# Kernel tuning notes

Measured on AMD Instinct MI355X. Metric: run time of the kernel, lower is better.

## Reference

```python
import jax, jax.numpy as jnp
import numpy as np
import math

B, T, N, D = 2, 2048, 16, 128


def setup_inputs() -> dict:
    key = jax.random.key(0)
    ks = jax.random.split(key, 9)
    s = 1.0 / math.sqrt(D)
    return {
        "x": jax.random.normal(ks[0], (B, T, N, D), dtype=jnp.float32),
        "wq": jax.random.normal(ks[1], (D, D), dtype=jnp.float32) * s,
        "bq": jax.random.normal(ks[2], (D,), dtype=jnp.float32) * 0.02,
        "wk": jax.random.normal(ks[3], (D, D), dtype=jnp.float32) * s,
        "bk": jax.random.normal(ks[4], (D,), dtype=jnp.float32) * 0.02,
        "wv": jax.random.normal(ks[5], (D, D), dtype=jnp.float32) * s,
        "bv": jax.random.normal(ks[6], (D,), dtype=jnp.float32) * 0.02,
        "wp": jax.random.normal(ks[7], (D, D), dtype=jnp.float32) * s,
        "bp": jax.random.normal(ks[8], (D,), dtype=jnp.float32) * 0.02,
    }


def reference(x, wq, bq, wk, bk, wv, bv, wp, bp):
    # x: (B, T, N, D); per-head Linear projections (torch y = x @ W.T + b)
    d = x.shape[-1]
    q = jnp.einsum("btnd,ed->btne", x, wq) + bq  # (B,T,N,D)
    k = jnp.einsum("btnd,ed->btne", x, wk) + bk
    v = jnp.einsum("btnd,ed->btne", x, wv) + bv
    scale = 1.0 / jnp.sqrt(jnp.asarray(d, dtype=x.dtype))
    # scores: (B, N, T, T)
    scores = jnp.einsum("btnd,bsnd->bnts", q, k) * scale
    t = scores.shape[-1]
    causal = jnp.tril(jnp.ones((t, t), dtype=bool))  # (T,T)
    scores = jnp.where(causal[None, None], scores, jnp.asarray(-jnp.inf, scores.dtype))
    w = jax.nn.softmax(scores, axis=-1)
    att = jnp.einsum("bnts,bsnd->btnd", w, v)  # (B,T,N,D)
    out = jnp.einsum("btnd,ed->btne", att, wp) + bp
    return out
```

## Files before the change

kernel.cpp:

```cpp
#include <hip/hip_runtime.h>
#include <cmath>

#define BB 2
#define TT 2048
#define NN 16
#define DD 128
#define NROWS (BB*TT*NN)
#define PLANE (TT*DD)
#define KP 132
#define VP 68

typedef unsigned short u16;
typedef unsigned int   u32;
typedef __attribute__((ext_vector_type(8)))  short s8v;
typedef __attribute__((ext_vector_type(16))) float vf16;

__device__ u16 g_Q [(size_t)NROWS * DD];
__device__ u16 g_K [(size_t)NROWS * DD];
__device__ u16 g_V [(size_t)NROWS * DD];
__device__ u16 g_VT[(size_t)NROWS * DD];

__device__ __forceinline__ u16 f2bf(float f) {
    return (u16)((__float_as_uint(f) + 0x8000u) >> 16);
}
__device__ __forceinline__ u32 pk2(float a, float b) {
    return ((__float_as_uint(a) + 0x8000u) >> 16)
         | ((__float_as_uint(b) + 0x8000u) & 0xFFFF0000u);
}
__device__ __forceinline__ void st8(u16* p, const float4& a, const float4& b) {
    uint2 lo, hi;
    lo.x = pk2(a.x, a.y); lo.y = pk2(a.z, a.w);
    hi.x = pk2(b.x, b.y); hi.y = pk2(b.z, b.w);
    *(uint2*)p       = lo;
    *(uint2*)(p + 4) = hi;
}
__device__ __forceinline__ s8v ld8(const u16* p) {
    short4 a = *(const short4*)p;
    short4 b = *(const short4*)(p + 4);
    return (s8v){a.x, a.y, a.z, a.w, b.x, b.y, b.z, b.w};
}

__global__ __launch_bounds__(256)
void qkv_proj_kernel(const float* __restrict__ x,
                     const float* __restrict__ Wq, const float* __restrict__ Bq,
                     const float* __restrict__ Wk, const float* __restrict__ Bk,
                     const float* __restrict__ Wv, const float* __restrict__ Bv)
{
    __shared__ u16 Xs[128*KP];
    __shared__ u16 Ws[128*KP];

    const int t  = threadIdx.x;
    const int r0 = blockIdx.x * 128;
    const float4* xsrc = (const float4*)(x + (size_t)r0*DD);

    #pragma unroll
    for (int it = 0; it < 8; ++it) {
        int i = t + 256*it;
        int e = i >> 4, c8 = i & 15;
        st8(&Xs[e*KP + c8*8], xsrc[2*i], xsrc[2*i + 1]);
    }
    #pragma unroll
    for (int it = 0; it < 8; ++it) {
        int i = t + 256*it;
        int e = i >> 4, c8 = i & 15;
        st8(&Ws[e*KP + c8*8], ((const float4*)Wq)[2*i], ((const float4*)Wq)[2*i + 1]);
    }
    __syncthreads();

    const int w   = t >> 6;
    const int l31 = t & 31;
    const int q2  = (t >> 5) & 1;

    s8v af[8];
    #pragma unroll
    for (int s = 0; s < 8; ++s)
        af[s] = ld8(&Xs[(w*32 + l31)*KP + s*16 + q2*8]);

    #pragma unroll
    for (int wsel = 0; wsel < 3; ++wsel) {
        const float* Bi = (wsel == 0) ? Bq : (wsel == 1) ? Bk : Bv;
        u16*         Ot = (wsel == 0) ? g_Q : (wsel == 1) ? g_K : g_V;

        vf16 acc[4];
        #pragma unroll
        for (int et = 0; et < 4; ++et)
            #pragma unroll
            for (int i = 0; i < 16; ++i) acc[et][i] = 0.f;

        #pragma unroll
        for (int s = 0; s < 8; ++s) {
            #pragma unroll
            for (int et = 0; et < 4; ++et) {
                s8v bf = ld8(&Ws[(et*32 + l31)*KP + s*16 + q2*8]);
                acc[et] = __builtin_amdgcn_mfma_f32_32x32x16_bf16(af[s], bf, acc[et], 0, 0, 0);
            }
        }

        float bb[4];
        #pragma unroll
        for (int et = 0; et < 4; ++et) bb[et] = Bi[et*32 + l31];

        #pragma unroll
        for (int r = 0; r < 16; ++r) {
            int rl = (r & 3) + 8*(r >> 2) + 4*q2;
            int rg = r0 + w*32 + rl;
            int b = rg >> 15, rem = rg & 32767;
            int tt = rem >> 4, n = rem & 15;
            size_t orow = (size_t)((b*NN + n)*TT + tt) * DD;
            #pragma unroll
            for (int et = 0; et < 4; ++et)
                Ot[orow + et*32 + l31] = f2bf(acc[et][r] + bb[et]);
        }

        if (wsel < 2) {
            const float* Wn = (wsel == 0) ? Wk : Wv;
            __syncthreads();
            #pragma unroll
            for (int it = 0; it < 8; ++it) {
                int i = t + 256*it;
                int e = i >> 4, c8 = i & 15;
                st8(&Ws[e*KP + c8*8], ((const float4*)Wn)[2*i], ((const float4*)Wn)[2*i + 1]);
            }
            __syncthreads();
        }
    }
}

__global__ __launch_bounds__(256)
void out_proj_kernel(const float* __restrict__ W, const float* __restrict__ Bi,
                     float* __restrict__ out)
{
    __shared__ u16 Ws[128*KP];

    const int t  = threadIdx.x;
    const int r0 = blockIdx.x * 128;

    #pragma unroll
    for (int it = 0; it < 8; ++it) {
        int i = t + 256*it;
        int e = i >> 4, c8 = i & 15;
        st8(&Ws[e*KP + c8*8], ((const float4*)W)[2*i], ((const float4*)W)[2*i + 1]);
    }

    const int w   = t >> 6;
    const int l31 = t & 31;
    const int q2  = (t >> 5) & 1;

    s8v af[8];
    {
        const u16* src = g_Q + (size_t)(r0 + w*32 + l31)*DD;
        #pragma unroll
        for (int s = 0; s < 8; ++s)
            af[s] = *(const s8v*)&src[s*16 + q2*8];
    }
    __syncthreads();

    vf16 acc[4];
    #pragma unroll
    for (int et = 0; et < 4; ++et)
        #pragma unroll
        for (int i = 0; i < 16; ++i) acc[et][i] = 0.f;

    #pragma unroll
    for (int s = 0; s < 8; ++s) {
        #pragma unroll
        for (int et = 0; et < 4; ++et) {
            s8v bf = ld8(&Ws[(et*32 + l31)*KP + s*16 + q2*8]);
            acc[et] = __builtin_amdgcn_mfma_f32_32x32x16_bf16(af[s], bf, acc[et], 0, 0, 0);
        }
    }

    float bb[4];
    #pragma unroll
    for (int et = 0; et < 4; ++et) bb[et] = Bi[et*32 + l31];

    #pragma unroll
    for (int r = 0; r < 16; ++r) {
        int rl = (r & 3) + 8*(r >> 2) + 4*q2;
        int rg = r0 + w*32 + rl;
        int b = rg >> 15, rem = rg & 32767;
        int n = rem >> 11, tt = rem & 2047;
        size_t orow = (size_t)((b*TT + tt)*NN + n) * DD;
        #pragma unroll
        for (int et = 0; et < 4; ++et)
            out[orow + et*32 + l31] = acc[et][r] + bb[et];
    }
}

__global__ __launch_bounds__(256)
void vtrans_kernel()
{
    const int t   = threadIdx.x;
    const int blk = blockIdx.x;
    const int pl  = blk >> 7;
    const int seg = blk & 127;
    const size_t plane = (size_t)pl * PLANE;
    const int w = t >> 6, lane = t & 63;
    const int d   = (w & 1)*64 + lane;
    const int tt0 = seg*16 + (w >> 1)*8;

    const u16* src = g_V + plane + (size_t)tt0*DD + d;
    u16 e[8];
    #pragma unroll
    for (int i = 0; i < 8; ++i) e[i] = src[(size_t)i*DD];
    uint4 pk;
    pk.x = (u32)e[0] | ((u32)e[1] << 16);
    pk.y = (u32)e[2] | ((u32)e[3] << 16);
    pk.z = (u32)e[4] | ((u32)e[5] << 16);
    pk.w = (u32)e[6] | ((u32)e[7] << 16);
    *(uint4*)&g_VT[plane + (size_t)d*TT + tt0] = pk;
}

__global__ __launch_bounds__(256, 2)
void attn_kernel()
{
    __shared__ u16 Ks[64*KP];
    __shared__ u16 Vt[128*VP];

    const int t   = threadIdx.x;
    const int grp = blockIdx.x >> 5;
    const int bn  = blockIdx.x & 31;
    const int qt  = (grp < 8) ? (15 - grp) : (grp - 8);
    const int q0  = qt * 128;
    const size_t plane = (size_t)bn * PLANE;
    const u16* Kg = g_K  + plane;
    const u16* Vg = g_VT + plane;

    const int w      = t >> 6;
    const int lane   = t & 63;
    const int lane31 = lane & 31;
    const int q2     = lane >> 5;
    const int qband  = q0 + 32*w;
    const int qrow   = qband + lane31;

    s8v qf[8];
    {
        const u16* Qg = g_Q + plane + (size_t)qrow * DD;
        #pragma unroll
        for (int s = 0; s < 8; ++s)
            qf[s] = *(const s8v*)&Qg[s*16 + q2*8];
    }

    vf16 accO[4];
    #pragma unroll
    for (int dt = 0; dt < 4; ++dt)
        #pragma unroll
        for (int i = 0; i < 16; ++i) accO[dt][i] = 0.f;

    float mrow = -INFINITY, lrow = 0.f;
    const float sc2 = 0.08838834764831845f * 1.4426950408889634f;

    const int nkt = 2*qt + 2;

    uint4 pk[4], pv[4];
    #pragma unroll
    for (int c = 0; c < 4; ++c) {
        int j = t + 256*c;
        int kr = j >> 4, kc = j & 15;
        pk[c] = *(const uint4*)&Kg[kr*DD + kc*8];
        int vr = j >> 3, vc = j & 7;
        pv[c] = *(const uint4*)&Vg[(size_t)vr*TT + vc*8];
    }

    for (int kt = 0; kt < nkt; ++kt) {
        const int k0 = kt*64;
        __syncthreads();
        #pragma unroll
        for (int c = 0; c < 4; ++c) {
            int j = t + 256*c;
            int kr = j >> 4, kc = j & 15;
            uint2 a, b;
            a.x = pk[c].x; a.y = pk[c].y; b.x = pk[c].z; b.y = pk[c].w;
            *(uint2*)&Ks[kr*KP + kc*8]     = a;
            *(uint2*)&Ks[kr*KP + kc*8 + 4] = b;
            int vr = j >> 3, vc = j & 7;
            a.x = pv[c].x; a.y = pv[c].y; b.x = pv[c].z; b.y = pv[c].w;
            *(uint2*)&Vt[vr*VP + vc*8]     = a;
            *(uint2*)&Vt[vr*VP + vc*8 + 4] = b;
        }
        __syncthreads();

        if (kt + 1 < nkt) {
            const u16* Kg2 = Kg + (size_t)(k0 + 64)*DD;
            const u16* Vg2 = Vg + (k0 + 64);
            #pragma unroll
            for (int c = 0; c < 4; ++c) {
                int j = t + 256*c;
                int kr = j >> 4, kc = j & 15;
                pk[c] = *(const uint4*)&Kg2[kr*DD + kc*8];
                int vr = j >> 3, vc = j & 7;
                pv[c] = *(const uint4*)&Vg2[(size_t)vr*TT + vc*8];
            }
        }

        if (k0 > qband + 31) continue;

        vf16 accS[2];
        #pragma unroll
        for (int kk = 0; kk < 2; ++kk)
            #pragma unroll
            for (int i = 0; i < 16; ++i) accS[kk][i] = 0.f;
        #pragma unroll
        for (int s = 0; s < 8; ++s) {
            #pragma unroll
            for (int kk = 0; kk < 2; ++kk) {
                s8v a = ld8(&Ks[(kk*32 + lane31)*KP + s*16 + q2*8]);
                accS[kk] = __builtin_amdgcn_mfma_f32_32x32x16_bf16(a, qf[s], accS[kk], 0, 0, 0);
            }
        }

        float p[2][16];
        const bool tail = (k0 + 63 > qband);
        #pragma unroll
        for (int kk = 0; kk < 2; ++kk)
            #pragma unroll
            for (int r = 0; r < 16; ++r) {
                float sv = accS[kk][r] * sc2;
                if (tail) {
                    int keyg = k0 + kk*32 + (r & 3) + 8*(r >> 2) + 4*q2;
                    if (keyg > qrow) sv = -INFINITY;
                }
                p[kk][r] = sv;
            }

        float vmax = -INFINITY;
        #pragma unroll
        for (int kk = 0; kk < 2; ++kk)
            #pragma unroll
            for (int r = 0; r < 16; ++r) vmax = fmaxf(vmax, p[kk][r]);
        vmax = fmaxf(vmax, __shfl_xor(vmax, 32));
        float mold = mrow;
        float mnew = fmaxf(mold, vmax);
        float alpha = __builtin_amdgcn_exp2f(mold - mnew);
        mrow = mnew;
        float ls = 0.f;
        #pragma unroll
        for (int kk = 0; kk < 2; ++kk)
            #pragma unroll
            for (int r = 0; r < 16; ++r) {
                float e = __builtin_amdgcn_exp2f(p[kk][r] - mnew);
                p[kk][r] = e;
                ls += e;
            }
        ls += __shfl_xor(ls, 32);
        lrow = lrow*alpha + ls;

        if (__any(mnew > mold)) {
            float ar[16];
            #pragma unroll
            for (int r = 0; r < 16; ++r)
                ar[r] = __shfl(alpha, (r & 3) + 8*(r >> 2) + 4*q2);
            #pragma unroll
            for (int dt = 0; dt < 4; ++dt)
                #pragma unroll
                for (int r = 0; r < 16; ++r) accO[dt][r] *= ar[r];
        }

        s8v pf[4];
        #pragma unroll
        for (int tau = 0; tau < 4; ++tau) {
            int kk = tau >> 1, rb = (tau & 1)*8;
            s8v v;
            #pragma unroll
            for (int j = 0; j < 8; ++j)
                v[j] = (short)(__float_as_uint(p[kk][rb + j]) >> 16);
            pf[tau] = v;
        }

        #pragma unroll
        for (int dt = 0; dt < 4; ++dt) {
            const u16* vp = &Vt[(dt*32 + lane31)*VP];
            #pragma unroll
            for (int tau = 0; tau < 4; ++tau) {
                const u16* q = vp + 16*tau + 4*q2;
                short4 lo = *(const short4*)q;
                short4 hi = *(const short4*)(q + 8);
                s8v bvv = {lo.x, lo.y, lo.z, lo.w, hi.x, hi.y, hi.z, hi.w};
                accO[dt] = __builtin_amdgcn_mfma_f32_32x32x16_bf16(pf[tau], bvv, accO[dt], 0, 0, 0);
            }
        }
    }

    float inv = 1.0f / lrow;
    #pragma unroll
    for (int r = 0; r < 16; ++r) {
        int rl = (r & 3) + 8*(r >> 2) + 4*q2;
        float ir = __shfl(inv, rl);
        u16* op = g_Q + plane + (size_t)(qband + rl)*DD;
        #pragma unroll
        for (int dt = 0; dt < 4; ++dt)
            op[dt*32 + lane31] = f2bf(accO[dt][r] * ir);
    }
}

extern "C" void kernel_launch(void* const* d_in, const int* in_sizes, int n_in,
                              void* d_out, int out_size, void* d_ws, size_t ws_size,
                              hipStream_t stream)
{
    const float* x  = (const float*)d_in[0];
    const float* wq = (const float*)d_in[1];
    const float* bq = (const float*)d_in[2];
    const float* wk = (const float*)d_in[3];
    const float* bk = (const float*)d_in[4];
    const float* wv = (const float*)d_in[5];
    const float* bv = (const float*)d_in[6];
    const float* wp = (const float*)d_in[7];
    const float* bp = (const float*)d_in[8];
    float* out = (float*)d_out;
    (void)d_ws; (void)ws_size;

    dim3 blk(256);
    qkv_proj_kernel<<<dim3(NROWS/128), blk, 0, stream>>>(
        x, wq, bq, wk, bk, wv, bv);
    vtrans_kernel<<<dim3(BB*NN*128), blk, 0, stream>>>();
    attn_kernel<<<dim3(BB*NN*(TT/128)), blk, 0, stream>>>();
    out_proj_kernel<<<dim3(NROWS/128), blk, 0, stream>>>(wp, bp, out);
}
```

Measured before the change: 208.0 us.

## Balance causal attention work with split-KV pairing, fuse V transpose, coalesce stores

Attention blocks now pair a heavy and a light query tile and split the heavy tile's KV range across two blocks, so every block does 17 KV tiles. Partial results (O, m, l) go to global scratch and a new combine kernel merges them. The V transpose moves into the QKV projection through shared memory, which removes a kernel and the g_V buffer. The Q/K and output projection stores are staged through LDS for coalesced writes. The trade-off is extra float partial traffic, an added launch for the combine step, and more LDS use in out_proj.

```diff
diff --git a/kernel.cpp b/kernel.cpp
--- a/kernel.cpp
+++ b/kernel.cpp
@@ -17,8 +17,10 @@
 
 __device__ u16 g_Q [(size_t)NROWS * DD];
 __device__ u16 g_K [(size_t)NROWS * DD];
-__device__ u16 g_V [(size_t)NROWS * DD];
 __device__ u16 g_VT[(size_t)NROWS * DD];
+__device__ float g_pO[2][256][128*128];
+__device__ float g_pm[2][256][128];
+__device__ float g_pl[2][256][128];
 
 __device__ __forceinline__ u16 f2bf(float f) {
     return (u16)((__float_as_uint(f) + 0x8000u) >> 16);
@@ -58,11 +60,6 @@
         int i = t + 256*it;
         int e = i >> 4, c8 = i & 15;
         st8(&Xs[e*KP + c8*8], xsrc[2*i], xsrc[2*i + 1]);
-    }
-    #pragma unroll
-    for (int it = 0; it < 8; ++it) {
-        int i = t + 256*it;
-        int e = i >> 4, c8 = i & 15;
         st8(&Ws[e*KP + c8*8], ((const float4*)Wq)[2*i], ((const float4*)Wq)[2*i + 1]);
     }
     __syncthreads();
@@ -79,7 +76,6 @@
     #pragma unroll
     for (int wsel = 0; wsel < 3; ++wsel) {
         const float* Bi = (wsel == 0) ? Bq : (wsel == 1) ? Bk : Bv;
-        u16*         Ot = (wsel == 0) ? g_Q : (wsel == 1) ? g_K : g_V;
 
         vf16 acc[4];
         #pragma unroll
@@ -100,16 +96,59 @@
         #pragma unroll
         for (int et = 0; et < 4; ++et) bb[et] = Bi[et*32 + l31];
 
-        #pragma unroll
-        for (int r = 0; r < 16; ++r) {
-            int rl = (r & 3) + 8*(r >> 2) + 4*q2;
-            int rg = r0 + w*32 + rl;
+        __syncthreads();
+        if (wsel < 2) {
+            #pragma unroll
+            for (int et = 0; et < 4; ++et)
+                #pragma unroll
+                for (int r = 0; r < 16; ++r) {
+                    int rl = (r & 3) + 8*(r >> 2) + 4*q2;
+                    Ws[(w*32 + rl)*KP + et*32 + l31] = f2bf(acc[et][r] + bb[et]);
+                }
+        } else {
+            #pragma unroll
+            for (int et = 0; et < 4; ++et)
+                #pragma unroll
+                for (int r = 0; r < 16; ++r) {
+                    int rl = (r & 3) + 8*(r >> 2) + 4*q2;
+                    Ws[(et*32 + l31)*KP + w*32 + rl] = f2bf(acc[et][r] + bb[et]);
+                }
+        }
+        __syncthreads();
+
+        if (wsel < 2) {
+            u16* Ot = (wsel == 0) ? g_Q : g_K;
+            int row = t >> 1, half = t & 1;
+            int rg = r0 + row;
             int b = rg >> 15, rem = rg & 32767;
             int tt = rem >> 4, n = rem & 15;
-            size_t orow = (size_t)((b*NN + n)*TT + tt) * DD;
-            #pragma unroll
-            for (int et = 0; et < 4; ++et)
-                Ot[orow + et*32 + l31] = f2bf(acc[et][r] + bb[et]);
+            u16* dst = Ot + (size_t)((b*NN + n)*TT + tt)*DD + half*64;
+            const u16* src = &Ws[row*KP + half*64];
+            #pragma unroll
+            for (int j = 0; j < 8; ++j) {
+                uint2 a = ((const uint2*)src)[2*j];
+                uint2 c = ((const uint2*)src)[2*j + 1];
+                uint4 v; v.x = a.x; v.y = a.y; v.z = c.x; v.w = c.y;
+                ((uint4*)dst)[j] = v;
+            }
+        } else {
+            int b  = r0 >> 15;
+            int t0 = (r0 & 32767) >> 4;
+            #pragma unroll
+            for (int it = 0; it < 8; ++it) {
+                int idx = t + 256*it;
+                int n = idx >> 7, d = idx & 127;
+                u16 e[8];
+                #pragma unroll
+                for (int ti = 0; ti < 8; ++ti)
+                    e[ti] = Ws[d*KP + ti*16 + n];
+                uint4 pkv;
+                pkv.x = (u32)e[0] | ((u32)e[1] << 16);
+                pkv.y = (u32)e[2] | ((u32)e[3] << 16);
+                pkv.z = (u32)e[4] | ((u32)e[5] << 16);
+                pkv.w = (u32)e[6] | ((u32)e[7] << 16);
+                *(uint4*)&g_VT[(size_t)(b*NN + n)*PLANE + (size_t)d*TT + t0] = pkv;
+            }
         }
 
         if (wsel < 2) {
@@ -130,7 +169,8 @@
 void out_proj_kernel(const float* __restrict__ W, const float* __restrict__ Bi,
                      float* __restrict__ out)
 {
-    __shared__ u16 Ws[128*KP];
+    __shared__ u16   Ws[128*KP];
+    __shared__ float Cs[128*66];
 
     const int t  = threadIdx.x;
     const int r0 = blockIdx.x * 128;
@@ -174,41 +214,36 @@
     #pragma unroll
     for (int et = 0; et < 4; ++et) bb[et] = Bi[et*32 + l31];
 
-    #pragma unroll
-    for (int r = 0; r < 16; ++r) {
-        int rl = (r & 3) + 8*(r >> 2) + 4*q2;
-        int rg = r0 + w*32 + rl;
-        int b = rg >> 15, rem = rg & 32767;
-        int n = rem >> 11, tt = rem & 2047;
-        size_t orow = (size_t)((b*TT + tt)*NN + n) * DD;
-        #pragma unroll
-        for (int et = 0; et < 4; ++et)
-            out[orow + et*32 + l31] = acc[et][r] + bb[et];
-    }
-}
-
-__global__ __launch_bounds__(256)
-void vtrans_kernel()
-{
-    const int t   = threadIdx.x;
-    const int blk = blockIdx.x;
-    const int pl  = blk >> 7;
-    const int seg = blk & 127;
-    const size_t plane = (size_t)pl * PLANE;
-    const int w = t >> 6, lane = t & 63;
-    const int d   = (w & 1)*64 + lane;
-    const int tt0 = seg*16 + (w >> 1)*8;
-
-    const u16* src = g_V + plane + (size_t)tt0*DD + d;
-    u16 e[8];
-    #pragma unroll
-    for (int i = 0; i < 8; ++i) e[i] = src[(size_t)i*DD];
-    uint4 pk;
-    pk.x = (u32)e[0] | ((u32)e[1] << 16);
-    pk.y = (u32)e[2] | ((u32)e[3] << 16);
-    pk.z = (u32)e[4] | ((u32)e[5] << 16);
-    pk.w = (u32)e[6] | ((u32)e[7] << 16);
-    *(uint4*)&g_VT[plane + (size_t)d*TT + tt0] = pk;
+    const int row  = t >> 1;
+    const int seg  = t & 1;
+    int rg = r0 + row;
+    int b = rg >> 15, rem = rg & 32767;
+    int n = rem >> 11, tt = rem & 2047;
+    float* orow = out + (size_t)((b*TT + tt)*NN + n)*DD;
+
+    #pragma unroll
+    for (int h = 0; h < 2; ++h) {
+        #pragma unroll
+        for (int e2 = 0; e2 < 2; ++e2) {
+            int et = 2*h + e2;
+            #pragma unroll
+            for (int r = 0; r < 16; ++r) {
+                int rl = (r & 3) + 8*(r >> 2) + 4*q2;
+                Cs[(w*32 + rl)*66 + e2*32 + l31] = acc[et][r] + bb[et];
+            }
+        }
+        __syncthreads();
+        {
+            const float* src = &Cs[row*66 + seg*32];
+            float* dst = orow + h*64 + seg*32;
+            #pragma unroll
+            for (int j = 0; j < 16; ++j) {
+                float2 v = ((const float2*)src)[j];
+                ((float2*)dst)[j] = v;
+            }
+        }
+        __syncthreads();
+    }
 }
 
 __global__ __launch_bounds__(256, 2)
@@ -217,11 +252,16 @@
     __shared__ u16 Ks[64*KP];
     __shared__ u16 Vt[128*VP];
 
-    const int t   = threadIdx.x;
-    const int grp = blockIdx.x >> 5;
-    const int bn  = blockIdx.x & 31;
-    const int qt  = (grp < 8) ? (15 - grp) : (grp - 8);
-    const int q0  = qt * 128;
+    const int t    = threadIdx.x;
+    const int pid  = blockIdx.x;
+    const int bn   = pid & 31;
+    const int sid  = (pid >> 5) & 1;
+    const int g    = pid >> 6;
+    const int qt_h = 15 - g;
+    const int nkt_h = 2*qt_h + 2;
+    const int qt_l = g;
+    const int hidx = g*32 + bn;
+
     const size_t plane = (size_t)bn * PLANE;
     const u16* Kg = g_K  + plane;
     const u16* Vg = g_VT + plane;
@@ -230,8 +270,9 @@
     const int lane   = t & 63;
     const int lane31 = lane & 31;
     const int q2     = lane >> 5;
-    const int qband  = q0 + 32*w;
-    const int qrow   = qband + lane31;
+
+    int qband = qt_h*128 + 32*w;
+    int qrow  = qband + lane31;
 
     s8v qf[8];
     {
@@ -250,20 +291,57 @@
     float mrow = -INFINITY, lrow = 0.f;
     const float sc2 = 0.08838834764831845f * 1.4426950408889634f;
 
-    const int nkt = 2*qt + 2;
+    const int ph1n = (sid == 0) ? 17 : (nkt_h - 17);
+
+    auto K0 = [&](int i) -> int {
+        if (sid == 0) return i*64;
+        return (i < ph1n) ? (17 + i)*64 : (i - ph1n)*64;
+    };
 
     uint4 pk[4], pv[4];
-    #pragma unroll
-    for (int c = 0; c < 4; ++c) {
-        int j = t + 256*c;
-        int kr = j >> 4, kc = j & 15;
-        pk[c] = *(const uint4*)&Kg[kr*DD + kc*8];
-        int vr = j >> 3, vc = j & 7;
-        pv[c] = *(const uint4*)&Vg[(size_t)vr*TT + vc*8];
-    }
-
-    for (int kt = 0; kt < nkt; ++kt) {
-        const int k0 = kt*64;
+    {
+        const u16* Kg2 = Kg + (size_t)K0(0)*DD;
+        const u16* Vg2 = Vg + K0(0);
+        #pragma unroll
+        for (int c = 0; c < 4; ++c) {
+            int j = t + 256*c;
+            int kr = j >> 4, kc = j & 15;
+            pk[c] = *(const uint4*)&Kg2[kr*DD + kc*8];
+            int vr = j >> 3, vc = j & 7;
+            pv[c] = *(const uint4*)&Vg2[(size_t)vr*TT + vc*8];
+        }
+    }
+
+    for (int i = 0; i < 17; ++i) {
+        const int k0 = K0(i);
+
+        if (sid == 1 && i == ph1n) {
+            if (lane < 32) {
+                g_pm[1][hidx][32*w + lane31] = mrow;
+                g_pl[1][hidx][32*w + lane31] = lrow;
+            }
+            float* po = &g_pO[1][hidx][0];
+            #pragma unroll
+            for (int r = 0; r < 16; ++r) {
+                int rl = (r & 3) + 8*(r >> 2) + 4*q2;
+                float* dst = po + (32*w + rl)*128;
+                #pragma unroll
+                for (int dt = 0; dt < 4; ++dt)
+                    dst[dt*32 + lane31] = accO[dt][r];
+            }
+            qband = qt_l*128 + 32*w;
+            qrow  = qband + lane31;
+            const u16* Qg = g_Q + plane + (size_t)qrow * DD;
+            #pragma unroll
+            for (int s = 0; s < 8; ++s)
+                qf[s] = *(const s8v*)&Qg[s*16 + q2*8];
+            #pragma unroll
+            for (int dt = 0; dt < 4; ++dt)
+                #pragma unroll
+                for (int r = 0; r < 16; ++r) accO[dt][r] = 0.f;
+            mrow = -INFINITY; lrow = 0.f;
+        }
+
         __syncthreads();
         #pragma unroll
         for (int c = 0; c < 4; ++c) {
@@ -280,9 +358,10 @@
         }
         __syncthreads();
 
-        if (kt + 1 < nkt) {
-            const u16* Kg2 = Kg + (size_t)(k0 + 64)*DD;
-            const u16* Vg2 = Vg + (k0 + 64);
+        if (i + 1 < 17) {
+            const int kn = K0(i + 1);
+            const u16* Kg2 = Kg + (size_t)kn*DD;
+            const u16* Vg2 = Vg + kn;
             #pragma unroll
             for (int c = 0; c < 4; ++c) {
                 int j = t + 256*c;
@@ -299,7 +378,7 @@
         #pragma unroll
         for (int kk = 0; kk < 2; ++kk)
             #pragma unroll
-            for (int i = 0; i < 16; ++i) accS[kk][i] = 0.f;
+            for (int i2 = 0; i2 < 16; ++i2) accS[kk][i2] = 0.f;
         #pragma unroll
         for (int s = 0; s < 8; ++s) {
             #pragma unroll
@@ -381,15 +460,68 @@
         }
     }
 
-    float inv = 1.0f / lrow;
-    #pragma unroll
-    for (int r = 0; r < 16; ++r) {
-        int rl = (r & 3) + 8*(r >> 2) + 4*q2;
-        float ir = __shfl(inv, rl);
-        u16* op = g_Q + plane + (size_t)(qband + rl)*DD;
-        #pragma unroll
-        for (int dt = 0; dt < 4; ++dt)
-            op[dt*32 + lane31] = f2bf(accO[dt][r] * ir);
+    if (sid == 0) {
+        if (lane < 32) {
+            g_pm[0][hidx][32*w + lane31] = mrow;
+            g_pl[0][hidx][32*w + lane31] = lrow;
+        }
+        float* po = &g_pO[0][hidx][0];
+        #pragma unroll
+        for (int r = 0; r < 16; ++r) {
+            int rl = (r & 3) + 8*(r >> 2) + 4*q2;
+            float* dst = po + (32*w + rl)*128;
+            #pragma unroll
+            for (int dt = 0; dt < 4; ++dt)
+                dst[dt*32 + lane31] = accO[dt][r];
+        }
+    } else {
+        float inv = 1.0f / lrow;
+        #pragma unroll
+        for (int r = 0; r < 16; ++r) {
+            int rl = (r & 3) + 8*(r >> 2) + 4*q2;
+            float ir = __shfl(inv, rl);
+            u16* op = g_Q + plane + (size_t)(qband + rl)*DD;
+            #pragma unroll
+            for (int dt = 0; dt < 4; ++dt)
+                op[dt*32 + lane31] = f2bf(accO[dt][r] * ir);
+        }
+    }
+}
+
+__global__ __launch_bounds__(256)
+void combine_kernel()
+{
+    const int hidx = blockIdx.x;
+    const int g    = hidx >> 5;
+    const int bn   = hidx & 31;
+    const int qt_h = 15 - g;
+
+    const int t    = threadIdx.x;
+    const int row  = t >> 1;
+    const int half = t & 1;
+
+    float m1 = g_pm[0][hidx][row], l1 = g_pl[0][hidx][row];
+    float m2 = g_pm[1][hidx][row], l2 = g_pl[1][hidx][row];
+    float m  = fmaxf(m1, m2);
+    float a1 = __builtin_amdgcn_exp2f(m1 - m);
+    float a2 = __builtin_amdgcn_exp2f(m2 - m);
+    float inv = 1.0f / (a1*l1 + a2*l2);
+    a1 *= inv; a2 *= inv;
+
+    const float* O1 = &g_pO[0][hidx][row*128 + half*64];
+    const float* O2 = &g_pO[1][hidx][row*128 + half*64];
+    u16* dst = g_Q + (size_t)bn*PLANE + (size_t)(qt_h*128 + row)*DD + half*64;
+
+    #pragma unroll
+    for (int j = 0; j < 16; ++j) {
+        float4 u = ((const float4*)O1)[j];
+        float4 v = ((const float4*)O2)[j];
+        float o0 = a1*u.x + a2*v.x;
+        float o1 = a1*u.y + a2*v.y;
+        float o2 = a1*u.z + a2*v.z;
+        float o3 = a1*u.w + a2*v.w;
+        uint2 pw; pw.x = pk2(o0, o1); pw.y = pk2(o2, o3);
+        ((uint2*)dst)[j] = pw;
     }
 }
 
@@ -412,7 +544,7 @@
     dim3 blk(256);
     qkv_proj_kernel<<<dim3(NROWS/128), blk, 0, stream>>>(
         x, wq, bq, wk, bk, wv, bv);
-    vtrans_kernel<<<dim3(BB*NN*128), blk, 0, stream>>>();
-    attn_kernel<<<dim3(BB*NN*(TT/128)), blk, 0, stream>>>();
+    attn_kernel<<<dim3(512), blk, 0, stream>>>();
+    combine_kernel<<<dim3(256), blk, 0, stream>>>();
     out_proj_kernel<<<dim3(NROWS/128), blk, 0, stream>>>(wp, bp, out);
 }
```

Result: slower. 233.9 us (+12.4%).
